# Kernel tuning notes

Hardware: AMD Instinct MI355X
Metric: run time of the kernel (lower is better)

The kernel has to match this reference:

```python
import jax, jax.numpy as jnp
import numpy as np

B, S, H, I = 2, 2048, 4096, 14336

def setup_inputs() -> dict:
    key = jax.random.key(0)
    k1, k2, k3, k4 = jax.random.split(key, 4)
    sH = 1.0 / np.sqrt(H)
    sI = 1.0 / np.sqrt(I)
    return {
        "x": jax.random.normal(k1, (B, S, H), dtype=jnp.float32),
        "w_gate": jax.random.normal(k2, (I, H), dtype=jnp.float32) * sH,
        "w_up": jax.random.normal(k3, (I, H), dtype=jnp.float32) * sH,
        "w_down": jax.random.normal(k4, (H, I), dtype=jnp.float32) * sI,
    }

def reference(x, w_gate, w_up, w_down):
    # SwiGLU gated MLP: down( silu(x @ Wg^T) * (x @ Wu^T) )
    g = jnp.einsum("bsh,ih->bsi", x, w_gate)   # [B,S,I]
    u = jnp.einsum("bsh,ih->bsi", x, w_up)     # [B,S,I]
    a = jax.nn.silu(g) * u                      # fused silu_mul
    d = jnp.einsum("bsi,hi->bsh", a, w_down)   # [B,S,H]
    return d
```

## Files before the change

kernel.cpp:

```cpp
#include <hip/hip_runtime.h>
#include <hip/hip_bf16.h>
#include <stdint.h>

typedef __bf16 bf16_t;
typedef __bf16 bf16x4 __attribute__((ext_vector_type(4)));
typedef __bf16 bf16x8 __attribute__((ext_vector_type(8)));
typedef float f32x4 __attribute__((ext_vector_type(4)));

#define LDS_CAST(p) ((__attribute__((address_space(3))) void*)(p))
#define GLB_CAST(p) ((const __attribute__((address_space(1))) void*)(p))

__device__ __forceinline__ void gl_lds16(const void* g, void* l) {
  __builtin_amdgcn_global_load_lds(GLB_CAST(g), LDS_CAST(l), 16, 0, 0);
}

#define MFMA16(a,b,c) __builtin_amdgcn_mfma_f32_16x16x32_bf16((a),(b),(c),0,0,0)
#define BARRIER() __builtin_amdgcn_s_barrier()

template<int N> __device__ __forceinline__ void vmw() {
  if constexpr (N == 8)      asm volatile("s_waitcnt vmcnt(8)" ::: "memory");
  else if constexpr (N == 6) asm volatile("s_waitcnt vmcnt(6)" ::: "memory");
  else if constexpr (N == 4) asm volatile("s_waitcnt vmcnt(4)" ::: "memory");
  else if constexpr (N == 0) asm volatile("s_waitcnt vmcnt(0)" ::: "memory");
}

static constexpr int M_TOT = 4096, H_DIM = 4096, I_DIM = 14336;

__global__ __launch_bounds__(256)
void k_conv(const float4* __restrict__ src, bf16x4* __restrict__ dst, long n4)
{
  long stride = (long)gridDim.x * blockDim.x;
  for (long i = (long)blockIdx.x * blockDim.x + threadIdx.x; i < n4; i += stride) {
    float4 v = src[i];
    bf16x4 o;
    o[0] = (bf16_t)v.x; o[1] = (bf16_t)v.y; o[2] = (bf16_t)v.z; o[3] = (bf16_t)v.w;
    dst[i] = o;
  }
}

__global__ __launch_bounds__(512, 2)
void k_gateup8(const bf16_t* __restrict__ X, const bf16_t* __restrict__ Wg,
               const bf16_t* __restrict__ Wu, bf16_t* __restrict__ Aout)
{
  __shared__ __align__(1024) char lds[131072];
  const int tid = threadIdx.x, wave = tid >> 6, lane = tid & 63;
  const int lr = lane & 15, kg = lane >> 4;
  const int xm = ((lr >> 3) & 1) << 5;
  const int wm = wave >> 2, wn = wave & 3;

  const int bid = blockIdx.x;
  const int i8  = bid >> 3;
  const int tn  = (bid & 7) * 14 + (i8 >> 4);
  const int tm  = i8 & 15;

  const int srow  = tid >> 2;
  const int scolb = ((tid & 3) * 16) ^ (((tid >> 5) & 1) << 5);

  const bf16_t* gX = X  + (size_t)(tm * 256 + srow) * H_DIM + (scolb >> 1);
  const bf16_t* gG = Wg + (size_t)(tn * 128 + srow) * H_DIM + (scolb >> 1);
  const bf16_t* gU = Wu + (size_t)(tn * 128 + srow) * H_DIM + (scolb >> 1);
  const size_t xh = (size_t)128 * H_DIM;

  const int ck   = (kg * 16) ^ xm;
  const int offA = (wm * 128 + lr) * 64 + ck;
  const int offG = 16384 + (wn * 32 + lr) * 64 + ck;
  const int offU = offG + 8192;

  const f32x4 vz = {0.f, 0.f, 0.f, 0.f};
  f32x4 accg[8][2], accu[8][2];
#pragma unroll
  for (int m = 0; m < 8; ++m)
#pragma unroll
    for (int n = 0; n < 2; ++n) { accg[m][n] = vz; accu[m][n] = vz; }

#pragma unroll
  for (int t = 0; t < 3; ++t) {
    char* lb = lds + t * 32768 + wave * 1024;
    gl_lds16(gX + t * 32,      lb);
    gl_lds16(gX + xh + t * 32, lb + 8192);
    gl_lds16(gG + t * 32,      lb + 16384);
    gl_lds16(gU + t * 32,      lb + 24576);
  }
  vmw<8>(); BARRIER();

#define G1_TILE(T, DO_STG, WAITN, DO_BAR)                                    \
  {                                                                          \
    const char* bb = lds + (((T) & 3) << 15);                                \
    if (DO_STG) {                                                            \
      char* sb = lds + ((((T) + 3) & 3) << 15) + wave * 1024;                \
      const int kc = ((T) + 3) * 32;                                         \
      gl_lds16(gX + kc,      sb);                                            \
      gl_lds16(gX + xh + kc, sb + 8192);                                     \
      gl_lds16(gG + kc,      sb + 16384);                                    \
      gl_lds16(gU + kc,      sb + 24576);                                    \
    }                                                                        \
    bf16x8 bg[2], bu[2], a[8];                                               \
    _Pragma("unroll") for (int n = 0; n < 2; ++n) {                          \
      bg[n] = *(const bf16x8*)(bb + offG + n * 1024);                        \
      bu[n] = *(const bf16x8*)(bb + offU + n * 1024); }                      \
    _Pragma("unroll") for (int f = 0; f < 8; ++f)                            \
      a[f] = *(const bf16x8*)(bb + offA + f * 1024);                         \
    __builtin_amdgcn_s_setprio(1);                                           \
    _Pragma("unroll") for (int m = 0; m < 8; ++m)                            \
    _Pragma("unroll") for (int n = 0; n < 2; ++n) {                          \
      accg[m][n] = MFMA16(a[m], bg[n], accg[m][n]);                          \
      accu[m][n] = MFMA16(a[m], bu[n], accu[m][n]); }                        \
    __builtin_amdgcn_s_setprio(0);                                           \
    vmw<WAITN>();                                                            \
    if (DO_BAR) BARRIER();                                                   \
  }

  const int NT = H_DIM / 32;
  for (int T = 0; T <= NT - 4; ++T)
    G1_TILE(T, true, 6, true);
  G1_TILE(NT - 3, false, 4, true);
  G1_TILE(NT - 2, false, 0, true);
  G1_TILE(NT - 1, false, 8 , false);
#undef G1_TILE

  const int r0 = tm * 256 + wm * 128 + kg * 4;
  const int c0 = tn * 128 + wn * 32 + lr;
#pragma unroll
  for (int m = 0; m < 8; ++m)
#pragma unroll
    for (int n = 0; n < 2; ++n)
#pragma unroll
      for (int e = 0; e < 4; ++e) {
        float g = accg[m][n][e];
        float u = accu[m][n][e];
        float s = g / (1.0f + __expf(-g));
        Aout[(size_t)(r0 + m * 16 + e) * I_DIM + c0 + n * 16] = (bf16_t)(s * u);
      }
}

__global__ __launch_bounds__(512, 2)
void k_down8(const bf16_t* __restrict__ Aa, const bf16_t* __restrict__ Wd,
             float* __restrict__ D)
{
  __shared__ __align__(1024) char lds[131072];
  const int tid = threadIdx.x, wave = tid >> 6, lane = tid & 63;
  const int lr = lane & 15, kg = lane >> 4;
  const int xm = ((lr >> 3) & 1) << 5;
  const int wm = wave >> 2, wn = wave & 3;

  const int bid = blockIdx.x;
  const int i8  = bid >> 3;
  const int tn  = (bid & 7) * 2 + (i8 >> 4);
  const int tm  = i8 & 15;

  const int srow  = tid >> 2;
  const int scolb = ((tid & 3) * 16) ^ (((tid >> 5) & 1) << 5);

  const bf16_t* gA = Aa + (size_t)(tm * 256 + srow) * I_DIM + (scolb >> 1);
  const bf16_t* gB = Wd + (size_t)(tn * 256 + srow) * I_DIM + (scolb >> 1);
  const size_t hI = (size_t)128 * I_DIM;

  const int ck   = (kg * 16) ^ xm;
  const int offA = (wm * 128 + lr) * 64 + ck;
  const int offB = 16384 + (wn * 64 + lr) * 64 + ck;

  const f32x4 vz = {0.f, 0.f, 0.f, 0.f};
  f32x4 acc[8][4];
#pragma unroll
  for (int m = 0; m < 8; ++m)
#pragma unroll
    for (int n = 0; n < 4; ++n) acc[m][n] = vz;

#pragma unroll
  for (int t = 0; t < 3; ++t) {
    char* lb = lds + t * 32768 + wave * 1024;
    gl_lds16(gA + t * 32,      lb);
    gl_lds16(gA + hI + t * 32, lb + 8192);
    gl_lds16(gB + t * 32,      lb + 16384);
    gl_lds16(gB + hI + t * 32, lb + 24576);
  }
  vmw<8>(); BARRIER();

#define G2_TILE(T, DO_STG, WAITN, DO_BAR)                                    \
  {                                                                          \
    const char* bb = lds + (((T) & 3) << 15);                                \
    if (DO_STG) {                                                            \
      char* sb = lds + ((((T) + 3) & 3) << 15) + wave * 1024;                \
      const int kc = ((T) + 3) * 32;                                         \
      gl_lds16(gA + kc,      sb);                                            \
      gl_lds16(gA + hI + kc, sb + 8192);                                     \
      gl_lds16(gB + kc,      sb + 16384);                                    \
      gl_lds16(gB + hI + kc, sb + 24576);                                    \
    }                                                                        \
    bf16x8 b[4], a[8];                                                       \
    _Pragma("unroll") for (int n = 0; n < 4; ++n)                            \
      b[n] = *(const bf16x8*)(bb + offB + n * 1024);                         \
    _Pragma("unroll") for (int f = 0; f < 8; ++f)                            \
      a[f] = *(const bf16x8*)(bb + offA + f * 1024);                         \
    __builtin_amdgcn_s_setprio(1);                                           \
    _Pragma("unroll") for (int m = 0; m < 8; ++m)                            \
    _Pragma("unroll") for (int n = 0; n < 4; ++n)                            \
      acc[m][n] = MFMA16(a[m], b[n], acc[m][n]);                             \
    __builtin_amdgcn_s_setprio(0);                                           \
    vmw<WAITN>();                                                            \
    if (DO_BAR) BARRIER();                                                   \
  }

  const int NT = I_DIM / 32;
  for (int T = 0; T <= NT - 4; ++T)
    G2_TILE(T, true, 6, true);
  G2_TILE(NT - 3, false, 4, true);
  G2_TILE(NT - 2, false, 0, true);
  G2_TILE(NT - 1, false, 8, false);
#undef G2_TILE

  const int r0 = tm * 256 + wm * 128 + kg * 4;
  const int c0 = tn * 256 + wn * 64 + lr;
#pragma unroll
  for (int m = 0; m < 8; ++m)
#pragma unroll
    for (int n = 0; n < 4; ++n)
#pragma unroll
      for (int e = 0; e < 4; ++e)
        D[(size_t)(r0 + m * 16 + e) * H_DIM + c0 + n * 16] = acc[m][n][e];
}

extern "C" void kernel_launch(void* const* d_in, const int* in_sizes, int n_in,
                              void* d_out, int out_size, void* d_ws, size_t ws_size,
                              hipStream_t stream) {
  const float* x  = (const float*)d_in[0];
  const float* wg = (const float*)d_in[1];
  const float* wu = (const float*)d_in[2];
  const float* wd = (const float*)d_in[3];
  float* out = (float*)d_out;

  const size_t A_BYTES = (size_t)M_TOT * I_DIM * 2;
  const size_t X_BYTES = (size_t)M_TOT * H_DIM * 2;
  const size_t W_BYTES = (size_t)I_DIM * H_DIM * 2;
  char* ws = (char*)d_ws;
  bf16_t* Ab  = (bf16_t*)(ws);
  bf16_t* Xb  = (bf16_t*)(ws + A_BYTES);
  bf16_t* Wgb = (bf16_t*)(ws + A_BYTES + X_BYTES);
  bf16_t* Wub = (bf16_t*)(ws + A_BYTES + X_BYTES + W_BYTES);
  bf16_t* Wdb = Wgb;

  const long nX = (long)M_TOT * H_DIM / 4;
  const long nW = (long)I_DIM * H_DIM / 4;

  k_conv<<<dim3(2048), dim3(256), 0, stream>>>((const float4*)x,  (bf16x4*)Xb,  nX);
  k_conv<<<dim3(2048), dim3(256), 0, stream>>>((const float4*)wg, (bf16x4*)Wgb, nW);
  k_conv<<<dim3(2048), dim3(256), 0, stream>>>((const float4*)wu, (bf16x4*)Wub, nW);

  k_gateup8<<<dim3(16 * 112), dim3(512), 0, stream>>>(Xb, Wgb, Wub, Ab);

  k_conv<<<dim3(2048), dim3(256), 0, stream>>>((const float4*)wd, (bf16x4*)Wdb, nW);

  k_down8<<<dim3(16 * 16), dim3(512), 0, stream>>>(Ab, Wdb, out);
}
```

Before: 1.439 ms.

## Switch both GEMMs to 32x32x16 MFMA with fragment-ordered LDS layout

Replaces the 16x16x32 bf16 MFMA tiles with 32x32x16 MFMA instructions in both the gate/up and down kernels. The global-to-LDS staging is reorganised so each wave writes 32-row by 8-column fragments that lanes can read back contiguously (lane*16 bytes), which drops the XOR swizzle. Larger MFMA tiles issue fewer instructions and LDS reads per FLOP. The trade-off is different LDS access and global load coalescing patterns, plus new epilogue row indexing.

Result: slower. 1.746 ms (+21.3%).

```diff
diff --git a/kernel.cpp b/kernel.cpp
--- a/kernel.cpp
+++ b/kernel.cpp
@@ -5,7 +5,7 @@
 typedef __bf16 bf16_t;
 typedef __bf16 bf16x4 __attribute__((ext_vector_type(4)));
 typedef __bf16 bf16x8 __attribute__((ext_vector_type(8)));
-typedef float f32x4 __attribute__((ext_vector_type(4)));
+typedef float f32x16 __attribute__((ext_vector_type(16)));
 
 #define LDS_CAST(p) ((__attribute__((address_space(3))) void*)(p))
 #define GLB_CAST(p) ((const __attribute__((address_space(1))) void*)(p))
@@ -14,7 +14,7 @@
   __builtin_amdgcn_global_load_lds(GLB_CAST(g), LDS_CAST(l), 16, 0, 0);
 }
 
-#define MFMA16(a,b,c) __builtin_amdgcn_mfma_f32_16x16x32_bf16((a),(b),(c),0,0,0)
+#define MFMA32(a,b,c) __builtin_amdgcn_mfma_f32_32x32x16_bf16((a),(b),(c),0,0,0)
 #define BARRIER() __builtin_amdgcn_s_barrier()
 
 template<int N> __device__ __forceinline__ void vmw() {
@@ -38,48 +38,44 @@
   }
 }
 
+
 __global__ __launch_bounds__(512, 2)
 void k_gateup8(const bf16_t* __restrict__ X, const bf16_t* __restrict__ Wg,
                const bf16_t* __restrict__ Wu, bf16_t* __restrict__ Aout)
 {
   __shared__ __align__(1024) char lds[131072];
   const int tid = threadIdx.x, wave = tid >> 6, lane = tid & 63;
-  const int lr = lane & 15, kg = lane >> 4;
-  const int xm = ((lr >> 3) & 1) << 5;
+  const int l31 = lane & 31, hi = lane >> 5;
   const int wm = wave >> 2, wn = wave & 3;
+  const int lb = lane * 16;
 
   const int bid = blockIdx.x;
-  const int i8  = bid >> 3;
-  const int tn  = (bid & 7) * 14 + (i8 >> 4);
-  const int tm  = i8 & 15;
-
-  const int srow  = tid >> 2;
-  const int scolb = ((tid & 3) * 16) ^ (((tid >> 5) & 1) << 5);
-
-  const bf16_t* gX = X  + (size_t)(tm * 256 + srow) * H_DIM + (scolb >> 1);
-  const bf16_t* gG = Wg + (size_t)(tn * 128 + srow) * H_DIM + (scolb >> 1);
-  const bf16_t* gU = Wu + (size_t)(tn * 128 + srow) * H_DIM + (scolb >> 1);
-  const size_t xh = (size_t)128 * H_DIM;
-
-  const int ck   = (kg * 16) ^ xm;
-  const int offA = (wm * 128 + lr) * 64 + ck;
-  const int offG = 16384 + (wn * 32 + lr) * 64 + ck;
-  const int offU = offG + 8192;
-
-  const f32x4 vz = {0.f, 0.f, 0.f, 0.f};
-  f32x4 accg[8][2], accu[8][2];
-#pragma unroll
-  for (int m = 0; m < 8; ++m)
-#pragma unroll
-    for (int n = 0; n < 2; ++n) { accg[m][n] = vz; accu[m][n] = vz; }
+  const int bq  = bid >> 3;
+  const int tn  = (bid & 7) * 14 + (bq >> 4);
+  const int tm  = bq & 15;
+
+  const int srg = wave >> 1;
+  const int skol = (wave & 1) * 16 + hi * 8;
+  const int srow = srg * 32 + l31;
+
+  const bf16_t* gX1 = X  + (size_t)(tm * 256 + srow) * H_DIM + skol;
+  const bf16_t* gX2 = gX1 + (size_t)128 * H_DIM;
+  const bf16_t* gG  = Wg + (size_t)(tn * 128 + srow) * H_DIM + skol;
+  const bf16_t* gU  = Wu + (size_t)(tn * 128 + srow) * H_DIM + skol;
+
+  f32x16 accg[4], accu[4];
+#pragma unroll
+  for (int m = 0; m < 4; ++m)
+#pragma unroll
+    for (int r = 0; r < 16; ++r) { accg[m][r] = 0.f; accu[m][r] = 0.f; }
 
 #pragma unroll
   for (int t = 0; t < 3; ++t) {
-    char* lb = lds + t * 32768 + wave * 1024;
-    gl_lds16(gX + t * 32,      lb);
-    gl_lds16(gX + xh + t * 32, lb + 8192);
-    gl_lds16(gG + t * 32,      lb + 16384);
-    gl_lds16(gU + t * 32,      lb + 24576);
+    char* sb = lds + t * 32768 + wave * 1024;
+    gl_lds16(gX1 + t * 32, sb);
+    gl_lds16(gX2 + t * 32, sb + 8192);
+    gl_lds16(gG  + t * 32, sb + 16384);
+    gl_lds16(gU  + t * 32, sb + 24576);
   }
   vmw<8>(); BARRIER();
 
@@ -89,22 +85,24 @@
     if (DO_STG) {                                                            \
       char* sb = lds + ((((T) + 3) & 3) << 15) + wave * 1024;                \
       const int kc = ((T) + 3) * 32;                                         \
-      gl_lds16(gX + kc,      sb);                                            \
-      gl_lds16(gX + xh + kc, sb + 8192);                                     \
-      gl_lds16(gG + kc,      sb + 16384);                                    \
-      gl_lds16(gU + kc,      sb + 24576);                                    \
+      gl_lds16(gX1 + kc, sb);                                                \
+      gl_lds16(gX2 + kc, sb + 8192);                                         \
+      gl_lds16(gG  + kc, sb + 16384);                                        \
+      gl_lds16(gU  + kc, sb + 24576);                                        \
     }                                                                        \
-    bf16x8 bg[2], bu[2], a[8];                                               \
-    _Pragma("unroll") for (int n = 0; n < 2; ++n) {                          \
-      bg[n] = *(const bf16x8*)(bb + offG + n * 1024);                        \
-      bu[n] = *(const bf16x8*)(bb + offU + n * 1024); }                      \
-    _Pragma("unroll") for (int f = 0; f < 8; ++f)                            \
-      a[f] = *(const bf16x8*)(bb + offA + f * 1024);                         \
+    bf16x8 a[4][2], bgv[2], buv[2];                                          \
+    _Pragma("unroll") for (int kf = 0; kf < 2; ++kf) {                       \
+      bgv[kf] = *(const bf16x8*)(bb + 16384 + (wn * 2 + kf) * 1024 + lb);    \
+      buv[kf] = *(const bf16x8*)(bb + 24576 + (wn * 2 + kf) * 1024 + lb); }  \
+    _Pragma("unroll") for (int m = 0; m < 4; ++m)                            \
+    _Pragma("unroll") for (int kf = 0; kf < 2; ++kf)                         \
+      a[m][kf] = *(const bf16x8*)(bb + ((wm * 4 + m) * 2 + kf) * 1024 + lb); \
     __builtin_amdgcn_s_setprio(1);                                           \
-    _Pragma("unroll") for (int m = 0; m < 8; ++m)                            \
-    _Pragma("unroll") for (int n = 0; n < 2; ++n) {                          \
-      accg[m][n] = MFMA16(a[m], bg[n], accg[m][n]);                          \
-      accu[m][n] = MFMA16(a[m], bu[n], accu[m][n]); }                        \
+    _Pragma("unroll") for (int m = 0; m < 4; ++m) {                          \
+      accg[m] = MFMA32(a[m][0], bgv[0], accg[m]);                            \
+      accg[m] = MFMA32(a[m][1], bgv[1], accg[m]);                            \
+      accu[m] = MFMA32(a[m][0], buv[0], accu[m]);                            \
+      accu[m] = MFMA32(a[m][1], buv[1], accu[m]); }                          \
     __builtin_amdgcn_s_setprio(0);                                           \
     vmw<WAITN>();                                                            \
     if (DO_BAR) BARRIER();                                                   \
@@ -115,22 +113,21 @@
     G1_TILE(T, true, 6, true);
   G1_TILE(NT - 3, false, 4, true);
   G1_TILE(NT - 2, false, 0, true);
-  G1_TILE(NT - 1, false, 8 , false);
+  G1_TILE(NT - 1, false, -1, false);
 #undef G1_TILE
 
-  const int r0 = tm * 256 + wm * 128 + kg * 4;
-  const int c0 = tn * 128 + wn * 32 + lr;
-#pragma unroll
-  for (int m = 0; m < 8; ++m)
-#pragma unroll
-    for (int n = 0; n < 2; ++n)
-#pragma unroll
-      for (int e = 0; e < 4; ++e) {
-        float g = accg[m][n][e];
-        float u = accu[m][n][e];
-        float s = g / (1.0f + __expf(-g));
-        Aout[(size_t)(r0 + m * 16 + e) * I_DIM + c0 + n * 16] = (bf16_t)(s * u);
-      }
+  const int r0 = tm * 256 + wm * 128 + 4 * hi;
+  const int c0 = tn * 128 + wn * 32 + l31;
+#pragma unroll
+  for (int m = 0; m < 4; ++m)
+#pragma unroll
+    for (int r = 0; r < 16; ++r) {
+      const int row = r0 + m * 32 + (r & 3) + 8 * (r >> 2);
+      float g = accg[m][r];
+      float u = accu[m][r];
+      float s = g / (1.0f + __expf(-g));
+      Aout[(size_t)row * I_DIM + c0] = (bf16_t)(s * u);
+    }
 }
 
 __global__ __launch_bounds__(512, 2)
@@ -139,40 +136,39 @@
 {
   __shared__ __align__(1024) char lds[131072];
   const int tid = threadIdx.x, wave = tid >> 6, lane = tid & 63;
-  const int lr = lane & 15, kg = lane >> 4;
-  const int xm = ((lr >> 3) & 1) << 5;
+  const int l31 = lane & 31, hi = lane >> 5;
   const int wm = wave >> 2, wn = wave & 3;
+  const int lb = lane * 16;
 
   const int bid = blockIdx.x;
-  const int i8  = bid >> 3;
-  const int tn  = (bid & 7) * 2 + (i8 >> 4);
-  const int tm  = i8 & 15;
-
-  const int srow  = tid >> 2;
-  const int scolb = ((tid & 3) * 16) ^ (((tid >> 5) & 1) << 5);
-
-  const bf16_t* gA = Aa + (size_t)(tm * 256 + srow) * I_DIM + (scolb >> 1);
-  const bf16_t* gB = Wd + (size_t)(tn * 256 + srow) * I_DIM + (scolb >> 1);
-  const size_t hI = (size_t)128 * I_DIM;
-
-  const int ck   = (kg * 16) ^ xm;
-  const int offA = (wm * 128 + lr) * 64 + ck;
-  const int offB = 16384 + (wn * 64 + lr) * 64 + ck;
-
-  const f32x4 vz = {0.f, 0.f, 0.f, 0.f};
-  f32x4 acc[8][4];
-#pragma unroll
-  for (int m = 0; m < 8; ++m)
-#pragma unroll
-    for (int n = 0; n < 4; ++n) acc[m][n] = vz;
+  const int bq  = bid >> 3;
+  const int tn  = (bid & 7) * 2 + (bq >> 4);
+  const int tm  = bq & 15;
+
+  const int srg = wave >> 1;
+  const int skol = (wave & 1) * 16 + hi * 8;
+  const int srow = srg * 32 + l31;
+
+  const bf16_t* gA1 = Aa + (size_t)(tm * 256 + srow) * I_DIM + skol;
+  const bf16_t* gA2 = gA1 + (size_t)128 * I_DIM;
+  const bf16_t* gB1 = Wd + (size_t)(tn * 256 + srow) * I_DIM + skol;
+  const bf16_t* gB2 = gB1 + (size_t)128 * I_DIM;
+
+  f32x16 acc[4][2];
+#pragma unroll
+  for (int m = 0; m < 4; ++m)
+#pragma unroll
+    for (int n = 0; n < 2; ++n)
+#pragma unroll
+      for (int r = 0; r < 16; ++r) acc[m][n][r] = 0.f;
 
 #pragma unroll
   for (int t = 0; t < 3; ++t) {
-    char* lb = lds + t * 32768 + wave * 1024;
-    gl_lds16(gA + t * 32,      lb);
-    gl_lds16(gA + hI + t * 32, lb + 8192);
-    gl_lds16(gB + t * 32,      lb + 16384);
-    gl_lds16(gB + hI + t * 32, lb + 24576);
+    char* sb = lds + t * 32768 + wave * 1024;
+    gl_lds16(gA1 + t * 32, sb);
+    gl_lds16(gA2 + t * 32, sb + 8192);
+    gl_lds16(gB1 + t * 32, sb + 16384);
+    gl_lds16(gB2 + t * 32, sb + 24576);
   }
   vmw<8>(); BARRIER();
 
@@ -182,20 +178,24 @@
     if (DO_STG) {                                                            \
       char* sb = lds + ((((T) + 3) & 3) << 15) + wave * 1024;                \
       const int kc = ((T) + 3) * 32;                                         \
-      gl_lds16(gA + kc,      sb);                                            \
-      gl_lds16(gA + hI + kc, sb + 8192);                                     \
-      gl_lds16(gB + kc,      sb + 16384);                                    \
-      gl_lds16(gB + hI + kc, sb + 24576);                                    \
+      gl_lds16(gA1 + kc, sb);                                                \
+      gl_lds16(gA2 + kc, sb + 8192);                                         \
+      gl_lds16(gB1 + kc, sb + 16384);                                        \
+      gl_lds16(gB2 + kc, sb + 24576);                                        \
     }                                                                        \
-    bf16x8 b[4], a[8];                                                       \
-    _Pragma("unroll") for (int n = 0; n < 4; ++n)                            \
-      b[n] = *(const bf16x8*)(bb + offB + n * 1024);                         \
-    _Pragma("unroll") for (int f = 0; f < 8; ++f)                            \
-      a[f] = *(const bf16x8*)(bb + offA + f * 1024);                         \
+    bf16x8 a[4][2], bv[2][2];                                                \
+    _Pragma("unroll") for (int n = 0; n < 2; ++n)                            \
+    _Pragma("unroll") for (int kf = 0; kf < 2; ++kf)                         \
+      bv[n][kf] = *(const bf16x8*)(bb + 16384 +                              \
+                    ((wn * 2 + n) * 2 + kf) * 1024 + lb);                    \
+    _Pragma("unroll") for (int m = 0; m < 4; ++m)                            \
+    _Pragma("unroll") for (int kf = 0; kf < 2; ++kf)                         \
+      a[m][kf] = *(const bf16x8*)(bb + ((wm * 4 + m) * 2 + kf) * 1024 + lb); \
     __builtin_amdgcn_s_setprio(1);                                           \
-    _Pragma("unroll") for (int m = 0; m < 8; ++m)                            \
-    _Pragma("unroll") for (int n = 0; n < 4; ++n)                            \
-      acc[m][n] = MFMA16(a[m], b[n], acc[m][n]);                             \
+    _Pragma("unroll") for (int m = 0; m < 4; ++m)                            \
+    _Pragma("unroll") for (int n = 0; n < 2; ++n) {                          \
+      acc[m][n] = MFMA32(a[m][0], bv[n][0], acc[m][n]);                      \
+      acc[m][n] = MFMA32(a[m][1], bv[n][1], acc[m][n]); }                    \
     __builtin_amdgcn_s_setprio(0);                                           \
     vmw<WAITN>();                                                            \
     if (DO_BAR) BARRIER();                                                   \
@@ -206,18 +206,20 @@
     G2_TILE(T, true, 6, true);
   G2_TILE(NT - 3, false, 4, true);
   G2_TILE(NT - 2, false, 0, true);
-  G2_TILE(NT - 1, false, 8, false);
+  G2_TILE(NT - 1, false, -1, false);
 #undef G2_TILE
 
-  const int r0 = tm * 256 + wm * 128 + kg * 4;
-  const int c0 = tn * 256 + wn * 64 + lr;
-#pragma unroll
-  for (int m = 0; m < 8; ++m)
-#pragma unroll
-    for (int n = 0; n < 4; ++n)
-#pragma unroll
-      for (int e = 0; e < 4; ++e)
-        D[(size_t)(r0 + m * 16 + e) * H_DIM + c0 + n * 16] = acc[m][n][e];
+  const int r0 = tm * 256 + wm * 128 + 4 * hi;
+  const int c0 = tn * 256 + wn * 64 + l31;
+#pragma unroll
+  for (int m = 0; m < 4; ++m)
+#pragma unroll
+    for (int n = 0; n < 2; ++n)
+#pragma unroll
+      for (int r = 0; r < 16; ++r) {
+        const int row = r0 + m * 32 + (r & 3) + 8 * (r >> 2);
+        D[(size_t)row * H_DIM + c0 + n * 32] = acc[m][n][r];
+      }
 }
 
 extern "C" void kernel_launch(void* const* d_in, const int* in_sizes, int n_in,
```

## Shrink GEMM tiles to 128x128 with 4-wave blocks and triple-buffered LDS

Applied to the files above, without the earlier changes.

Both GEMM kernels go from 8-wave blocks with 256-row tiles and a 4-deep LDS ring to 4-wave blocks with 128x128 tiles and a 3-deep ring. Each wave now stages its own rows. The down-projection grid grows from 256 to 1024 blocks, which is meant to fill all CUs instead of leaving many idle, and the launch bounds allow more resident blocks. The cost is lower arithmetic intensity per tile and more global and L2 traffic. The prefetch depth also drops by one stage, and the last tile waits with vmcnt -1, which the vmw helper treats as a no-op.

Result: slower. 1.840 ms (+27.8%).

```diff
diff --git a/kernel.cpp b/kernel.cpp
--- a/kernel.cpp
+++ b/kernel.cpp
@@ -18,8 +18,7 @@
 #define BARRIER() __builtin_amdgcn_s_barrier()
 
 template<int N> __device__ __forceinline__ void vmw() {
-  if constexpr (N == 8)      asm volatile("s_waitcnt vmcnt(8)" ::: "memory");
-  else if constexpr (N == 6) asm volatile("s_waitcnt vmcnt(6)" ::: "memory");
+  if constexpr (N == 6)      asm volatile("s_waitcnt vmcnt(6)" ::: "memory");
   else if constexpr (N == 4) asm volatile("s_waitcnt vmcnt(4)" ::: "memory");
   else if constexpr (N == 0) asm volatile("s_waitcnt vmcnt(0)" ::: "memory");
 }
@@ -38,92 +37,88 @@
   }
 }
 
-__global__ __launch_bounds__(512, 2)
-void k_gateup8(const bf16_t* __restrict__ X, const bf16_t* __restrict__ Wg,
+__global__ __launch_bounds__(256, 2)
+void k_gateup4(const bf16_t* __restrict__ X, const bf16_t* __restrict__ Wg,
                const bf16_t* __restrict__ Wu, bf16_t* __restrict__ Aout)
 {
-  __shared__ __align__(1024) char lds[131072];
+  __shared__ __align__(1024) char lds[3 * 24576];
   const int tid = threadIdx.x, wave = tid >> 6, lane = tid & 63;
   const int lr = lane & 15, kg = lane >> 4;
-  const int xm = ((lr >> 3) & 1) << 5;
-  const int wm = wave >> 2, wn = wave & 3;
+  const int wm = wave >> 1, wn = wave & 1;
 
   const int bid = blockIdx.x;
-  const int i8  = bid >> 3;
-  const int tn  = (bid & 7) * 14 + (i8 >> 4);
-  const int tm  = i8 & 15;
-
-  const int srow  = tid >> 2;
-  const int scolb = ((tid & 3) * 16) ^ (((tid >> 5) & 1) << 5);
-
-  const bf16_t* gX = X  + (size_t)(tm * 256 + srow) * H_DIM + (scolb >> 1);
-  const bf16_t* gG = Wg + (size_t)(tn * 128 + srow) * H_DIM + (scolb >> 1);
-  const bf16_t* gU = Wu + (size_t)(tn * 128 + srow) * H_DIM + (scolb >> 1);
-  const size_t xh = (size_t)128 * H_DIM;
-
-  const int ck   = (kg * 16) ^ xm;
-  const int offA = (wm * 128 + lr) * 64 + ck;
-  const int offG = 16384 + (wn * 32 + lr) * 64 + ck;
-  const int offU = offG + 8192;
+  const int bq  = bid >> 3;
+  const int tn  = (bid & 7) * 14 + (bq >> 5);
+  const int tm  = bq & 31;
+
+  const int sr16  = lane >> 2;
+  const int scolb = ((lane & 3) * 16) ^ (((lane >> 5) & 1) << 5);
+
+  const bf16_t* gXw = X  + (size_t)(tm * 128 + wave * 32 + sr16) * H_DIM + (scolb >> 1);
+  const bf16_t* gGw = Wg + (size_t)(tn * 128 + wave * 32 + sr16) * H_DIM + (scolb >> 1);
+  const bf16_t* gUw = Wu + (size_t)(tn * 128 + wave * 32 + sr16) * H_DIM + (scolb >> 1);
+  const size_t rstep = (size_t)16 * H_DIM;
+
+  const int ck   = (kg * 16) ^ (((lr >> 3) & 1) << 5);
+  const int offA = (wm * 64 + lr) * 64 + ck;
+  const int offG = 8192  + (wn * 64 + lr) * 64 + ck;
+  const int offU = 16384 + (wn * 64 + lr) * 64 + ck;
 
   const f32x4 vz = {0.f, 0.f, 0.f, 0.f};
-  f32x4 accg[8][2], accu[8][2];
-#pragma unroll
-  for (int m = 0; m < 8; ++m)
-#pragma unroll
-    for (int n = 0; n < 2; ++n) { accg[m][n] = vz; accu[m][n] = vz; }
-
-#pragma unroll
-  for (int t = 0; t < 3; ++t) {
-    char* lb = lds + t * 32768 + wave * 1024;
-    gl_lds16(gX + t * 32,      lb);
-    gl_lds16(gX + xh + t * 32, lb + 8192);
-    gl_lds16(gG + t * 32,      lb + 16384);
-    gl_lds16(gU + t * 32,      lb + 24576);
-  }
-  vmw<8>(); BARRIER();
-
-#define G1_TILE(T, DO_STG, WAITN, DO_BAR)                                    \
-  {                                                                          \
-    const char* bb = lds + (((T) & 3) << 15);                                \
-    if (DO_STG) {                                                            \
-      char* sb = lds + ((((T) + 3) & 3) << 15) + wave * 1024;                \
-      const int kc = ((T) + 3) * 32;                                         \
-      gl_lds16(gX + kc,      sb);                                            \
-      gl_lds16(gX + xh + kc, sb + 8192);                                     \
-      gl_lds16(gG + kc,      sb + 16384);                                    \
-      gl_lds16(gU + kc,      sb + 24576);                                    \
-    }                                                                        \
-    bf16x8 bg[2], bu[2], a[8];                                               \
-    _Pragma("unroll") for (int n = 0; n < 2; ++n) {                          \
-      bg[n] = *(const bf16x8*)(bb + offG + n * 1024);                        \
-      bu[n] = *(const bf16x8*)(bb + offU + n * 1024); }                      \
-    _Pragma("unroll") for (int f = 0; f < 8; ++f)                            \
-      a[f] = *(const bf16x8*)(bb + offA + f * 1024);                         \
+  f32x4 accg[4][4], accu[4][4];
+#pragma unroll
+  for (int m = 0; m < 4; ++m)
+#pragma unroll
+    for (int n = 0; n < 4; ++n) { accg[m][n] = vz; accu[m][n] = vz; }
+
+#define G1_STAGE(dst, kc)                                                    \
+  { char* d_ = (dst) + wave * 2048;                                          \
+    gl_lds16(gXw + (kc),         d_);                                        \
+    gl_lds16(gXw + rstep + (kc), d_ + 1024);                                 \
+    gl_lds16(gGw + (kc),         d_ + 8192);                                 \
+    gl_lds16(gGw + rstep + (kc), d_ + 9216);                                 \
+    gl_lds16(gUw + (kc),         d_ + 16384);                                \
+    gl_lds16(gUw + rstep + (kc), d_ + 17408); }
+
+#define G1_TILE(bb, WAITN, DO_BAR)                                           \
+  { bf16x8 a[4], bg[4], bu[4];                                               \
+    _Pragma("unroll") for (int f = 0; f < 4; ++f) {                          \
+      a[f]  = *(const bf16x8*)((bb) + offA + f * 1024);                      \
+      bg[f] = *(const bf16x8*)((bb) + offG + f * 1024);                      \
+      bu[f] = *(const bf16x8*)((bb) + offU + f * 1024); }                    \
     __builtin_amdgcn_s_setprio(1);                                           \
-    _Pragma("unroll") for (int m = 0; m < 8; ++m)                            \
-    _Pragma("unroll") for (int n = 0; n < 2; ++n) {                          \
+    _Pragma("unroll") for (int m = 0; m < 4; ++m)                            \
+    _Pragma("unroll") for (int n = 0; n < 4; ++n) {                          \
       accg[m][n] = MFMA16(a[m], bg[n], accg[m][n]);                          \
       accu[m][n] = MFMA16(a[m], bu[n], accu[m][n]); }                        \
     __builtin_amdgcn_s_setprio(0);                                           \
     vmw<WAITN>();                                                            \
-    if (DO_BAR) BARRIER();                                                   \
+    if (DO_BAR) BARRIER(); }
+
+  char* B0 = lds; char* B1 = lds + 24576; char* B2 = lds + 49152;
+  G1_STAGE(B0, 0);
+  G1_STAGE(B1, 32);
+  vmw<6>(); BARRIER();
+
+  char *p_prev = B2, *p_cur = B0, *p_next = B1;
+  const int NT = H_DIM / 32;
+  for (int T = 0; T <= NT - 3; ++T) {
+    G1_STAGE(p_prev, (T + 2) * 32);
+    G1_TILE(p_cur, 6, true);
+    char* t_ = p_prev; p_prev = p_cur; p_cur = p_next; p_next = t_;
   }
-
-  const int NT = H_DIM / 32;
-  for (int T = 0; T <= NT - 4; ++T)
-    G1_TILE(T, true, 6, true);
-  G1_TILE(NT - 3, false, 4, true);
-  G1_TILE(NT - 2, false, 0, true);
-  G1_TILE(NT - 1, false, 8 , false);
+  G1_TILE(p_cur, 0, true);
+  { char* t_ = p_cur; p_cur = p_next; p_next = t_; }
+  G1_TILE(p_cur, -1, false);
 #undef G1_TILE
-
-  const int r0 = tm * 256 + wm * 128 + kg * 4;
-  const int c0 = tn * 128 + wn * 32 + lr;
-#pragma unroll
-  for (int m = 0; m < 8; ++m)
-#pragma unroll
-    for (int n = 0; n < 2; ++n)
+#undef G1_STAGE
+
+  const int r0 = tm * 128 + wm * 64 + kg * 4;
+  const int c0 = tn * 128 + wn * 64 + lr;
+#pragma unroll
+  for (int m = 0; m < 4; ++m)
+#pragma unroll
+    for (int n = 0; n < 4; ++n)
 #pragma unroll
       for (int e = 0; e < 4; ++e) {
         float g = accg[m][n][e];
@@ -133,86 +128,80 @@
       }
 }
 
-__global__ __launch_bounds__(512, 2)
-void k_down8(const bf16_t* __restrict__ Aa, const bf16_t* __restrict__ Wd,
+__global__ __launch_bounds__(256, 3)
+void k_down4(const bf16_t* __restrict__ Aa, const bf16_t* __restrict__ Wd,
              float* __restrict__ D)
 {
-  __shared__ __align__(1024) char lds[131072];
+  __shared__ __align__(1024) char lds[3 * 16384];
   const int tid = threadIdx.x, wave = tid >> 6, lane = tid & 63;
   const int lr = lane & 15, kg = lane >> 4;
-  const int xm = ((lr >> 3) & 1) << 5;
-  const int wm = wave >> 2, wn = wave & 3;
+  const int wm = wave >> 1, wn = wave & 1;
 
   const int bid = blockIdx.x;
-  const int i8  = bid >> 3;
-  const int tn  = (bid & 7) * 2 + (i8 >> 4);
-  const int tm  = i8 & 15;
-
-  const int srow  = tid >> 2;
-  const int scolb = ((tid & 3) * 16) ^ (((tid >> 5) & 1) << 5);
-
-  const bf16_t* gA = Aa + (size_t)(tm * 256 + srow) * I_DIM + (scolb >> 1);
-  const bf16_t* gB = Wd + (size_t)(tn * 256 + srow) * I_DIM + (scolb >> 1);
-  const size_t hI = (size_t)128 * I_DIM;
-
-  const int ck   = (kg * 16) ^ xm;
-  const int offA = (wm * 128 + lr) * 64 + ck;
-  const int offB = 16384 + (wn * 64 + lr) * 64 + ck;
+  const int bq  = bid >> 3;
+  const int tn  = (bid & 7) * 4 + (bq >> 5);
+  const int tm  = bq & 31;
+
+  const int sr16  = lane >> 2;
+  const int scolb = ((lane & 3) * 16) ^ (((lane >> 5) & 1) << 5);
+
+  const bf16_t* gAw = Aa + (size_t)(tm * 128 + wave * 32 + sr16) * I_DIM + (scolb >> 1);
+  const bf16_t* gBw = Wd + (size_t)(tn * 128 + wave * 32 + sr16) * I_DIM + (scolb >> 1);
+  const size_t rstep = (size_t)16 * I_DIM;
+
+  const int ck   = (kg * 16) ^ (((lr >> 3) & 1) << 5);
+  const int offA = (wm * 64 + lr) * 64 + ck;
+  const int offB = 8192 + (wn * 64 + lr) * 64 + ck;
 
   const f32x4 vz = {0.f, 0.f, 0.f, 0.f};
-  f32x4 acc[8][4];
-#pragma unroll
-  for (int m = 0; m < 8; ++m)
+  f32x4 acc[4][4];
+#pragma unroll
+  for (int m = 0; m < 4; ++m)
 #pragma unroll
     for (int n = 0; n < 4; ++n) acc[m][n] = vz;
 
-#pragma unroll
-  for (int t = 0; t < 3; ++t) {
-    char* lb = lds + t * 32768 + wave * 1024;
-    gl_lds16(gA + t * 32,      lb);
-    gl_lds16(gA + hI + t * 32, lb + 8192);
-    gl_lds16(gB + t * 32,      lb + 16384);
-    gl_lds16(gB + hI + t * 32, lb + 24576);
-  }
-  vmw<8>(); BARRIER();
-
-#define G2_TILE(T, DO_STG, WAITN, DO_BAR)                                    \
-  {                                                                          \
-    const char* bb = lds + (((T) & 3) << 15);                                \
-    if (DO_STG) {                                                            \
-      char* sb = lds + ((((T) + 3) & 3) << 15) + wave * 1024;                \
-      const int kc = ((T) + 3) * 32;                                         \
-      gl_lds16(gA + kc,      sb);                                            \
-      gl_lds16(gA + hI + kc, sb + 8192);                                     \
-      gl_lds16(gB + kc,      sb + 16384);                                    \
-      gl_lds16(gB + hI + kc, sb + 24576);                                    \
-    }                                                                        \
-    bf16x8 b[4], a[8];                                                       \
-    _Pragma("unroll") for (int n = 0; n < 4; ++n)                            \
-      b[n] = *(const bf16x8*)(bb + offB + n * 1024);                         \
-    _Pragma("unroll") for (int f = 0; f < 8; ++f)                            \
-      a[f] = *(const bf16x8*)(bb + offA + f * 1024);                         \
+#define G2_STAGE(dst, kc)                                                    \
+  { char* d_ = (dst) + wave * 2048;                                          \
+    gl_lds16(gAw + (kc),         d_);                                        \
+    gl_lds16(gAw + rstep + (kc), d_ + 1024);                                 \
+    gl_lds16(gBw + (kc),         d_ + 8192);                                 \
+    gl_lds16(gBw + rstep + (kc), d_ + 9216); }
+
+#define G2_TILE(bb, WAITN, DO_BAR)                                           \
+  { bf16x8 a[4], b[4];                                                       \
+    _Pragma("unroll") for (int f = 0; f < 4; ++f) {                          \
+      a[f] = *(const bf16x8*)((bb) + offA + f * 1024);                       \
+      b[f] = *(const bf16x8*)((bb) + offB + f * 1024); }                     \
     __builtin_amdgcn_s_setprio(1);                                           \
-    _Pragma("unroll") for (int m = 0; m < 8; ++m)                            \
+    _Pragma("unroll") for (int m = 0; m < 4; ++m)                            \
     _Pragma("unroll") for (int n = 0; n < 4; ++n)                            \
       acc[m][n] = MFMA16(a[m], b[n], acc[m][n]);                             \
     __builtin_amdgcn_s_setprio(0);                                           \
     vmw<WAITN>();                                                            \
-    if (DO_BAR) BARRIER();                                                   \
+    if (DO_BAR) BARRIER(); }
+
+  char* B0 = lds; char* B1 = lds + 16384; char* B2 = lds + 32768;
+  G2_STAGE(B0, 0);
+  G2_STAGE(B1, 32);
+  vmw<4>(); BARRIER();
+
+  char *p_prev = B2, *p_cur = B0, *p_next = B1;
+  const int NT = I_DIM / 32;
+  for (int T = 0; T <= NT - 3; ++T) {
+    G2_STAGE(p_prev, (T + 2) * 32);
+    G2_TILE(p_cur, 4, true);
+    char* t_ = p_prev; p_prev = p_cur; p_cur = p_next; p_next = t_;
   }
-
-  const int NT = I_DIM / 32;
-  for (int T = 0; T <= NT - 4; ++T)
-    G2_TILE(T, true, 6, true);
-  G2_TILE(NT - 3, false, 4, true);
-  G2_TILE(NT - 2, false, 0, true);
-  G2_TILE(NT - 1, false, 8, false);
+  G2_TILE(p_cur, 0, true);
+  { char* t_ = p_cur; p_cur = p_next; p_next = t_; }
+  G2_TILE(p_cur, -1, false);
 #undef G2_TILE
-
-  const int r0 = tm * 256 + wm * 128 + kg * 4;
-  const int c0 = tn * 256 + wn * 64 + lr;
-#pragma unroll
-  for (int m = 0; m < 8; ++m)
+#undef G2_STAGE
+
+  const int r0 = tm * 128 + wm * 64 + kg * 4;
+  const int c0 = tn * 128 + wn * 64 + lr;
+#pragma unroll
+  for (int m = 0; m < 4; ++m)
 #pragma unroll
     for (int n = 0; n < 4; ++n)
 #pragma unroll
@@ -246,9 +235,9 @@
   k_conv<<<dim3(2048), dim3(256), 0, stream>>>((const float4*)wg, (bf16x4*)Wgb, nW);
   k_conv<<<dim3(2048), dim3(256), 0, stream>>>((const float4*)wu, (bf16x4*)Wub, nW);
 
-  k_gateup8<<<dim3(16 * 112), dim3(512), 0, stream>>>(Xb, Wgb, Wub, Ab);
+  k_gateup4<<<dim3(32 * 112), dim3(256), 0, stream>>>(Xb, Wgb, Wub, Ab);
 
   k_conv<<<dim3(2048), dim3(256), 0, stream>>>((const float4*)wd, (bf16x4*)Wdb, nW);
 
-  k_down8<<<dim3(16 * 16), dim3(512), 0, stream>>>(Ab, Wdb, out);
-}
+  k_down4<<<dim3(32 * 32), dim3(256), 0, stream>>>(Ab, Wdb, out);
+}
```

## Restructure GEMM mainloops into double-buffered 64-K tiles with interleaved quarter-phase pipelining

Applied to the files above, without the earlier changes.

Both GEMM kernels move from a 4-stage ring of 32-wide K tiles to two 64-wide K buffers. Each K step is split into four phases, and each phase issues part of the next tile's global-to-LDS loads, reads half the A fragments, then runs MFMAs between barriers. This is the HipKittens-style 8-wave ping-pong schedule. It aims to overlap LDS reads, global loads and MFMA work more finely and to hold fewer fragment registers at once. In exchange it adds more barriers per K step and less prefetch depth in flight.

New measurement: 1.450 ms. No clear change (+0.7%).

```diff
diff --git a/kernel.cpp b/kernel.cpp
--- a/kernel.cpp
+++ b/kernel.cpp
@@ -16,11 +16,12 @@
 
 #define MFMA16(a,b,c) __builtin_amdgcn_mfma_f32_16x16x32_bf16((a),(b),(c),0,0,0)
 #define BARRIER() __builtin_amdgcn_s_barrier()
+#define LGKM0()  asm volatile("s_waitcnt lgkmcnt(0)" ::: "memory")
+#define PRIO(n)  __builtin_amdgcn_s_setprio(n)
 
 template<int N> __device__ __forceinline__ void vmw() {
-  if constexpr (N == 8)      asm volatile("s_waitcnt vmcnt(8)" ::: "memory");
-  else if constexpr (N == 6) asm volatile("s_waitcnt vmcnt(6)" ::: "memory");
-  else if constexpr (N == 4) asm volatile("s_waitcnt vmcnt(4)" ::: "memory");
+  if constexpr (N == 4)      asm volatile("s_waitcnt vmcnt(4)" ::: "memory");
+  else if constexpr (N == 2) asm volatile("s_waitcnt vmcnt(2)" ::: "memory");
   else if constexpr (N == 0) asm volatile("s_waitcnt vmcnt(0)" ::: "memory");
 }
 
@@ -47,11 +48,12 @@
   const int lr = lane & 15, kg = lane >> 4;
   const int xm = ((lr >> 3) & 1) << 5;
   const int wm = wave >> 2, wn = wave & 3;
+  const int wb = wave * 1024;
 
   const int bid = blockIdx.x;
-  const int i8  = bid >> 3;
-  const int tn  = (bid & 7) * 14 + (i8 >> 4);
-  const int tm  = i8 & 15;
+  const int bq  = bid >> 3;
+  const int tn  = (bid & 7) * 14 + (bq >> 4);
+  const int tm  = bq & 15;
 
   const int srow  = tid >> 2;
   const int scolb = ((tid & 3) * 16) ^ (((tid >> 5) & 1) << 5);
@@ -63,8 +65,7 @@
 
   const int ck   = (kg * 16) ^ xm;
   const int offA = (wm * 128 + lr) * 64 + ck;
-  const int offG = 16384 + (wn * 32 + lr) * 64 + ck;
-  const int offU = offG + 8192;
+  const int offG = (wn * 32 + lr) * 64 + ck;
 
   const f32x4 vz = {0.f, 0.f, 0.f, 0.f};
   f32x4 accg[8][2], accu[8][2];
@@ -73,50 +74,157 @@
 #pragma unroll
     for (int n = 0; n < 2; ++n) { accg[m][n] = vz; accu[m][n] = vz; }
 
-#pragma unroll
-  for (int t = 0; t < 3; ++t) {
-    char* lb = lds + t * 32768 + wave * 1024;
-    gl_lds16(gX + t * 32,      lb);
-    gl_lds16(gX + xh + t * 32, lb + 8192);
-    gl_lds16(gG + t * 32,      lb + 16384);
-    gl_lds16(gU + t * 32,      lb + 24576);
+  gl_lds16(gX,           lds + 0     + wb);
+  gl_lds16(gX + xh,      lds + 8192  + wb);
+  gl_lds16(gG,           lds + 32768 + wb);
+  gl_lds16(gU,           lds + 49152 + wb);
+  gl_lds16(gX + 32,      lds + 16384 + wb);
+  gl_lds16(gX + xh + 32, lds + 24576 + wb);
+  gl_lds16(gG + 32,      lds + 40960 + wb);
+  gl_lds16(gU + 32,      lds + 57344 + wb);
+  vmw<4>(); BARRIER();
+
+  const int NT = H_DIM / 64;
+  for (int T = 0; T <= NT - 2; ++T) {
+    const char* bb = lds + (T & 1) * 65536;
+    char* sb = lds + ((T + 1) & 1) * 65536 + wb;
+    const bf16_t* gXn = gX + (T + 1) * 64;
+    const bf16_t* gGn = gG + (T + 1) * 64;
+    const bf16_t* gUn = gU + (T + 1) * 64;
+    bf16x8 bg0, bg1, bu0, bu1;
+    {
+      bf16x8 a[4];
+#pragma unroll
+      for (int f = 0; f < 4; ++f) a[f] = *(const bf16x8*)(bb + offA + f * 1024);
+      bg0 = *(const bf16x8*)(bb + 32768 + offG);
+      bg1 = *(const bf16x8*)(bb + 32768 + offG + 1024);
+      bu0 = *(const bf16x8*)(bb + 49152 + offG);
+      bu1 = *(const bf16x8*)(bb + 49152 + offG + 1024);
+      gl_lds16(gXn, sb); gl_lds16(gXn + xh, sb + 8192);
+      BARRIER(); LGKM0();
+      PRIO(1);
+#pragma unroll
+      for (int m = 0; m < 4; ++m) {
+        accg[m][0] = MFMA16(a[m], bg0, accg[m][0]);
+        accg[m][1] = MFMA16(a[m], bg1, accg[m][1]);
+        accu[m][0] = MFMA16(a[m], bu0, accu[m][0]);
+        accu[m][1] = MFMA16(a[m], bu1, accu[m][1]);
+      }
+      PRIO(0);
+      vmw<4>(); BARRIER();
+    }
+    {
+      bf16x8 a[4];
+#pragma unroll
+      for (int f = 0; f < 4; ++f) a[f] = *(const bf16x8*)(bb + offA + (f + 4) * 1024);
+      gl_lds16(gGn, sb + 32768); gl_lds16(gUn, sb + 49152);
+      BARRIER(); LGKM0();
+      PRIO(1);
+#pragma unroll
+      for (int m = 0; m < 4; ++m) {
+        accg[4 + m][0] = MFMA16(a[m], bg0, accg[4 + m][0]);
+        accg[4 + m][1] = MFMA16(a[m], bg1, accg[4 + m][1]);
+        accu[4 + m][0] = MFMA16(a[m], bu0, accu[4 + m][0]);
+        accu[4 + m][1] = MFMA16(a[m], bu1, accu[4 + m][1]);
+      }
+      PRIO(0);
+      vmw<4>(); BARRIER();
+    }
+    {
+      bf16x8 a[4];
+#pragma unroll
+      for (int f = 0; f < 4; ++f) a[f] = *(const bf16x8*)(bb + 16384 + offA + f * 1024);
+      bg0 = *(const bf16x8*)(bb + 40960 + offG);
+      bg1 = *(const bf16x8*)(bb + 40960 + offG + 1024);
+      bu0 = *(const bf16x8*)(bb + 57344 + offG);
+      bu1 = *(const bf16x8*)(bb + 57344 + offG + 1024);
+      gl_lds16(gXn + 32, sb + 16384); gl_lds16(gXn + xh + 32, sb + 24576);
+      BARRIER(); LGKM0();
+      PRIO(1);
+#pragma unroll
+      for (int m = 0; m < 4; ++m) {
+        accg[m][0] = MFMA16(a[m], bg0, accg[m][0]);
+        accg[m][1] = MFMA16(a[m], bg1, accg[m][1]);
+        accu[m][0] = MFMA16(a[m], bu0, accu[m][0]);
+        accu[m][1] = MFMA16(a[m], bu1, accu[m][1]);
+      }
+      PRIO(0);
+      vmw<4>(); BARRIER();
+    }
+    {
+      bf16x8 a[4];
+#pragma unroll
+      for (int f = 0; f < 4; ++f) a[f] = *(const bf16x8*)(bb + 16384 + offA + (f + 4) * 1024);
+      gl_lds16(gGn + 32, sb + 40960); gl_lds16(gUn + 32, sb + 57344);
+      BARRIER(); LGKM0();
+      PRIO(1);
+#pragma unroll
+      for (int m = 0; m < 4; ++m) {
+        accg[4 + m][0] = MFMA16(a[m], bg0, accg[4 + m][0]);
+        accg[4 + m][1] = MFMA16(a[m], bg1, accg[4 + m][1]);
+        accu[4 + m][0] = MFMA16(a[m], bu0, accu[4 + m][0]);
+        accu[4 + m][1] = MFMA16(a[m], bu1, accu[4 + m][1]);
+      }
+      PRIO(0);
+      vmw<4>(); BARRIER();
+    }
   }
-  vmw<8>(); BARRIER();
-
-#define G1_TILE(T, DO_STG, WAITN, DO_BAR)                                    \
-  {                                                                          \
-    const char* bb = lds + (((T) & 3) << 15);                                \
-    if (DO_STG) {                                                            \
-      char* sb = lds + ((((T) + 3) & 3) << 15) + wave * 1024;                \
-      const int kc = ((T) + 3) * 32;                                         \
-      gl_lds16(gX + kc,      sb);                                            \
-      gl_lds16(gX + xh + kc, sb + 8192);                                     \
-      gl_lds16(gG + kc,      sb + 16384);                                    \
-      gl_lds16(gU + kc,      sb + 24576);                                    \
-    }                                                                        \
-    bf16x8 bg[2], bu[2], a[8];                                               \
-    _Pragma("unroll") for (int n = 0; n < 2; ++n) {                          \
-      bg[n] = *(const bf16x8*)(bb + offG + n * 1024);                        \
-      bu[n] = *(const bf16x8*)(bb + offU + n * 1024); }                      \
-    _Pragma("unroll") for (int f = 0; f < 8; ++f)                            \
-      a[f] = *(const bf16x8*)(bb + offA + f * 1024);                         \
-    __builtin_amdgcn_s_setprio(1);                                           \
-    _Pragma("unroll") for (int m = 0; m < 8; ++m)                            \
-    _Pragma("unroll") for (int n = 0; n < 2; ++n) {                          \
-      accg[m][n] = MFMA16(a[m], bg[n], accg[m][n]);                          \
-      accu[m][n] = MFMA16(a[m], bu[n], accu[m][n]); }                        \
-    __builtin_amdgcn_s_setprio(0);                                           \
-    vmw<WAITN>();                                                            \
-    if (DO_BAR) BARRIER();                                                   \
+  {
+    const char* bb = lds + ((NT - 1) & 1) * 65536;
+    bf16x8 bg0, bg1, bu0, bu1;
+    { bf16x8 a[4];
+#pragma unroll
+      for (int f = 0; f < 4; ++f) a[f] = *(const bf16x8*)(bb + offA + f * 1024);
+      bg0 = *(const bf16x8*)(bb + 32768 + offG);
+      bg1 = *(const bf16x8*)(bb + 32768 + offG + 1024);
+      bu0 = *(const bf16x8*)(bb + 49152 + offG);
+      bu1 = *(const bf16x8*)(bb + 49152 + offG + 1024);
+      BARRIER(); LGKM0(); PRIO(1);
+#pragma unroll
+      for (int m = 0; m < 4; ++m) {
+        accg[m][0] = MFMA16(a[m], bg0, accg[m][0]);
+        accg[m][1] = MFMA16(a[m], bg1, accg[m][1]);
+        accu[m][0] = MFMA16(a[m], bu0, accu[m][0]);
+        accu[m][1] = MFMA16(a[m], bu1, accu[m][1]); }
+      PRIO(0); vmw<2>(); BARRIER(); }
+    { bf16x8 a[4];
+#pragma unroll
+      for (int f = 0; f < 4; ++f) a[f] = *(const bf16x8*)(bb + offA + (f + 4) * 1024);
+      BARRIER(); LGKM0(); PRIO(1);
+#pragma unroll
+      for (int m = 0; m < 4; ++m) {
+        accg[4 + m][0] = MFMA16(a[m], bg0, accg[4 + m][0]);
+        accg[4 + m][1] = MFMA16(a[m], bg1, accg[4 + m][1]);
+        accu[4 + m][0] = MFMA16(a[m], bu0, accu[4 + m][0]);
+        accu[4 + m][1] = MFMA16(a[m], bu1, accu[4 + m][1]); }
+      PRIO(0); vmw<0>(); BARRIER(); }
+    { bf16x8 a[4];
+#pragma unroll
+      for (int f = 0; f < 4; ++f) a[f] = *(const bf16x8*)(bb + 16384 + offA + f * 1024);
+      bg0 = *(const bf16x8*)(bb + 40960 + offG);
+      bg1 = *(const bf16x8*)(bb + 40960 + offG + 1024);
+      bu0 = *(const bf16x8*)(bb + 57344 + offG);
+      bu1 = *(const bf16x8*)(bb + 57344 + offG + 1024);
+      LGKM0(); PRIO(1);
+#pragma unroll
+      for (int m = 0; m < 4; ++m) {
+        accg[m][0] = MFMA16(a[m], bg0, accg[m][0]);
+        accg[m][1] = MFMA16(a[m], bg1, accg[m][1]);
+        accu[m][0] = MFMA16(a[m], bu0, accu[m][0]);
+        accu[m][1] = MFMA16(a[m], bu1, accu[m][1]); }
+      PRIO(0); }
+    { bf16x8 a[4];
+#pragma unroll
+      for (int f = 0; f < 4; ++f) a[f] = *(const bf16x8*)(bb + 16384 + offA + (f + 4) * 1024);
+      LGKM0(); PRIO(1);
+#pragma unroll
+      for (int m = 0; m < 4; ++m) {
+        accg[4 + m][0] = MFMA16(a[m], bg0, accg[4 + m][0]);
+        accg[4 + m][1] = MFMA16(a[m], bg1, accg[4 + m][1]);
+        accu[4 + m][0] = MFMA16(a[m], bu0, accu[4 + m][0]);
+        accu[4 + m][1] = MFMA16(a[m], bu1, accu[4 + m][1]); }
+      PRIO(0); }
   }
-
-  const int NT = H_DIM / 32;
-  for (int T = 0; T <= NT - 4; ++T)
-    G1_TILE(T, true, 6, true);
-  G1_TILE(NT - 3, false, 4, true);
-  G1_TILE(NT - 2, false, 0, true);
-  G1_TILE(NT - 1, false, 8 , false);
-#undef G1_TILE
 
   const int r0 = tm * 256 + wm * 128 + kg * 4;
   const int c0 = tn * 128 + wn * 32 + lr;
@@ -142,11 +250,12 @@
   const int lr = lane & 15, kg = lane >> 4;
   const int xm = ((lr >> 3) & 1) << 5;
   const int wm = wave >> 2, wn = wave & 3;
+  const int wb = wave * 1024;
 
   const int bid = blockIdx.x;
-  const int i8  = bid >> 3;
-  const int tn  = (bid & 7) * 2 + (i8 >> 4);
-  const int tm  = i8 & 15;
+  const int bq  = bid >> 3;
+  const int tn  = (bid & 7) * 2 + (bq >> 4);
+  const int tm  = bq & 15;
 
   const int srow  = tid >> 2;
   const int scolb = ((tid & 3) * 16) ^ (((tid >> 5) & 1) << 5);
@@ -157,7 +266,7 @@
 
   const int ck   = (kg * 16) ^ xm;
   const int offA = (wm * 128 + lr) * 64 + ck;
-  const int offB = 16384 + (wn * 64 + lr) * 64 + ck;
+  const int offB = (wn * 64 + lr) * 64 + ck;
 
   const f32x4 vz = {0.f, 0.f, 0.f, 0.f};
   f32x4 acc[8][4];
@@ -166,48 +275,128 @@
 #pragma unroll
     for (int n = 0; n < 4; ++n) acc[m][n] = vz;
 
-#pragma unroll
-  for (int t = 0; t < 3; ++t) {
-    char* lb = lds + t * 32768 + wave * 1024;
-    gl_lds16(gA + t * 32,      lb);
-    gl_lds16(gA + hI + t * 32, lb + 8192);
-    gl_lds16(gB + t * 32,      lb + 16384);
-    gl_lds16(gB + hI + t * 32, lb + 24576);
+  gl_lds16(gA,           lds + 0     + wb);
+  gl_lds16(gA + hI,      lds + 8192  + wb);
+  gl_lds16(gB,           lds + 32768 + wb);
+  gl_lds16(gB + hI,      lds + 40960 + wb);
+  gl_lds16(gA + 32,      lds + 16384 + wb);
+  gl_lds16(gA + hI + 32, lds + 24576 + wb);
+  gl_lds16(gB + 32,      lds + 49152 + wb);
+  gl_lds16(gB + hI + 32, lds + 57344 + wb);
+  vmw<4>(); BARRIER();
+
+  const int NT = I_DIM / 64;
+  for (int T = 0; T <= NT - 2; ++T) {
+    const char* bb = lds + (T & 1) * 65536;
+    char* sb = lds + ((T + 1) & 1) * 65536 + wb;
+    const bf16_t* gAn = gA + (T + 1) * 64;
+    const bf16_t* gBn = gB + (T + 1) * 64;
+    bf16x8 bv[4];
+    {
+      bf16x8 a[4];
+#pragma unroll
+      for (int f = 0; f < 4; ++f) a[f] = *(const bf16x8*)(bb + offA + f * 1024);
+#pragma unroll
+      for (int n = 0; n < 4; ++n) bv[n] = *(const bf16x8*)(bb + 32768 + offB + n * 1024);
+      gl_lds16(gAn, sb); gl_lds16(gAn + hI, sb + 8192);
+      BARRIER(); LGKM0();
+      PRIO(1);
+#pragma unroll
+      for (int m = 0; m < 4; ++m)
+#pragma unroll
+        for (int n = 0; n < 4; ++n) acc[m][n] = MFMA16(a[m], bv[n], acc[m][n]);
+      PRIO(0);
+      vmw<4>(); BARRIER();
+    }
+    {
+      bf16x8 a[4];
+#pragma unroll
+      for (int f = 0; f < 4; ++f) a[f] = *(const bf16x8*)(bb + offA + (f + 4) * 1024);
+      gl_lds16(gBn, sb + 32768); gl_lds16(gBn + hI, sb + 40960);
+      BARRIER(); LGKM0();
+      PRIO(1);
+#pragma unroll
+      for (int m = 0; m < 4; ++m)
+#pragma unroll
+        for (int n = 0; n < 4; ++n) acc[4 + m][n] = MFMA16(a[m], bv[n], acc[4 + m][n]);
+      PRIO(0);
+      vmw<4>(); BARRIER();
+    }
+    {
+      bf16x8 a[4];
+#pragma unroll
+      for (int f = 0; f < 4; ++f) a[f] = *(const bf16x8*)(bb + 16384 + offA + f * 1024);
+#pragma unroll
+      for (int n = 0; n < 4; ++n) bv[n] = *(const bf16x8*)(bb + 49152 + offB + n * 1024);
+      gl_lds16(gAn + 32, sb + 16384); gl_lds16(gAn + hI + 32, sb + 24576);
+      BARRIER(); LGKM0();
+      PRIO(1);
+#pragma unroll
+      for (int m = 0; m < 4; ++m)
+#pragma unroll
+        for (int n = 0; n < 4; ++n) acc[m][n] = MFMA16(a[m], bv[n], acc[m][n]);
+      PRIO(0);
+      vmw<4>(); BARRIER();
+    }
+    {
+      bf16x8 a[4];
+#pragma unroll
+      for (int f = 0; f < 4; ++f) a[f] = *(const bf16x8*)(bb + 16384 + offA + (f + 4) * 1024);
+      gl_lds16(gBn + 32, sb + 49152); gl_lds16(gBn + hI + 32, sb + 57344);
+      BARRIER(); LGKM0();
+      PRIO(1);
+#pragma unroll
+      for (int m = 0; m < 4; ++m)
+#pragma unroll
+        for (int n = 0; n < 4; ++n) acc[4 + m][n] = MFMA16(a[m], bv[n], acc[4 + m][n]);
+      PRIO(0);
+      vmw<4>(); BARRIER();
+    }
   }
-  vmw<8>(); BARRIER();
-
-#define G2_TILE(T, DO_STG, WAITN, DO_BAR)                                    \
-  {                                                                          \
-    const char* bb = lds + (((T) & 3) << 15);                                \
-    if (DO_STG) {                                                            \
-      char* sb = lds + ((((T) + 3) & 3) << 15) + wave * 1024;                \
-      const int kc = ((T) + 3) * 32;                                         \
-      gl_lds16(gA + kc,      sb);                                            \
-      gl_lds16(gA + hI + kc, sb + 8192);                                     \
-      gl_lds16(gB + kc,      sb + 16384);                                    \
-      gl_lds16(gB + hI + kc, sb + 24576);                                    \
-    }                                                                        \
-    bf16x8 b[4], a[8];                                                       \
-    _Pragma("unroll") for (int n = 0; n < 4; ++n)                            \
-      b[n] = *(const bf16x8*)(bb + offB + n * 1024);                         \
-    _Pragma("unroll") for (int f = 0; f < 8; ++f)                            \
-      a[f] = *(const bf16x8*)(bb + offA + f * 1024);                         \
-    __builtin_amdgcn_s_setprio(1);                                           \
-    _Pragma("unroll") for (int m = 0; m < 8; ++m)                            \
-    _Pragma("unroll") for (int n = 0; n < 4; ++n)                            \
-      acc[m][n] = MFMA16(a[m], b[n], acc[m][n]);                             \
-    __builtin_amdgcn_s_setprio(0);                                           \
-    vmw<WAITN>();                                                            \
-    if (DO_BAR) BARRIER();                                                   \
+  {
+    const char* bb = lds + ((NT - 1) & 1) * 65536;
+    bf16x8 bv[4];
+    { bf16x8 a[4];
+#pragma unroll
+      for (int f = 0; f < 4; ++f) a[f] = *(const bf16x8*)(bb + offA + f * 1024);
+#pragma unroll
+      for (int n = 0; n < 4; ++n) bv[n] = *(const bf16x8*)(bb + 32768 + offB + n * 1024);
+      BARRIER(); LGKM0(); PRIO(1);
+#pragma unroll
+      for (int m = 0; m < 4; ++m)
+#pragma unroll
+        for (int n = 0; n < 4; ++n) acc[m][n] = MFMA16(a[m], bv[n], acc[m][n]);
+      PRIO(0); vmw<2>(); BARRIER(); }
+    { bf16x8 a[4];
+#pragma unroll
+      for (int f = 0; f < 4; ++f) a[f] = *(const bf16x8*)(bb + offA + (f + 4) * 1024);
+      BARRIER(); LGKM0(); PRIO(1);
+#pragma unroll
+      for (int m = 0; m < 4; ++m)
+#pragma unroll
+        for (int n = 0; n < 4; ++n) acc[4 + m][n] = MFMA16(a[m], bv[n], acc[4 + m][n]);
+      PRIO(0); vmw<0>(); BARRIER(); }
+    { bf16x8 a[4];
+#pragma unroll
+      for (int f = 0; f < 4; ++f) a[f] = *(const bf16x8*)(bb + 16384 + offA + f * 1024);
+#pragma unroll
+      for (int n = 0; n < 4; ++n) bv[n] = *(const bf16x8*)(bb + 49152 + offB + n * 1024);
+      LGKM0(); PRIO(1);
+#pragma unroll
+      for (int m = 0; m < 4; ++m)
+#pragma unroll
+        for (int n = 0; n < 4; ++n) acc[m][n] = MFMA16(a[m], bv[n], acc[m][n]);
+      PRIO(0); }
+    { bf16x8 a[4];
+#pragma unroll
+      for (int f = 0; f < 4; ++f) a[f] = *(const bf16x8*)(bb + 16384 + offA + (f + 4) * 1024);
+      LGKM0(); PRIO(1);
+#pragma unroll
+      for (int m = 0; m < 4; ++m)
+#pragma unroll
+        for (int n = 0; n < 4; ++n) acc[4 + m][n] = MFMA16(a[m], bv[n], acc[4 + m][n]);
+      PRIO(0); }
   }
-
-  const int NT = I_DIM / 32;
-  for (int T = 0; T <= NT - 4; ++T)
-    G2_TILE(T, true, 6, true);
-  G2_TILE(NT - 3, false, 4, true);
-  G2_TILE(NT - 2, false, 0, true);
-  G2_TILE(NT - 1, false, 8, false);
-#undef G2_TILE
 
   const int r0 = tm * 256 + wm * 128 + kg * 4;
   const int c0 = tn * 256 + wn * 64 + lr;
```
